# Performance work log

Hardware: AMD Instinct MI355X
Metric: run time of the kernel (lower is better)

Reference implementation:

```python
import jax, jax.numpy as jnp
import numpy as np

D_MODEL = 512
NUM_HEADS = 8
LN_EPS = 1e-5


def _linear(x, W, b):
    # torch nn.Linear: y = x @ W.T + b, W is [out, in]
    return x @ W.T + b


def _layernorm(x, g, b):
    mu = jnp.mean(x, axis=-1, keepdims=True)
    var = jnp.mean((x - mu) ** 2, axis=-1, keepdims=True)
    return (x - mu) * jax.lax.rsqrt(var + LN_EPS) * g + b


def _proj_block(x, W1, b1, ln_g, ln_b, W2, b2):
    # Linear -> LayerNorm -> GELU(exact) -> Linear
    h = _linear(x, W1, b1)
    h = _layernorm(h, ln_g, ln_b)
    h = jax.nn.gelu(h, approximate=False)
    return _linear(h, W2, b2)


def setup_inputs() -> dict:
    key = jax.random.key(0)
    ks = jax.random.split(key, 16)
    d = D_MODEL
    B, N = 32, 50000
    s = 0.02
    inp = {
        "query_features": jax.random.normal(ks[0], (B, d), jnp.float32),
        "candidate_features": jax.random.normal(ks[1], (N, d), jnp.float32),
        # temperature param init: log(1/0.07)
        "temperature": jnp.asarray(np.log(1.0 / 0.07), jnp.float32),
        # query projection
        "qW1": jax.random.normal(ks[2], (d, d), jnp.float32) * s,
        "qb1": jnp.zeros((d,), jnp.float32),
        "q_ln_g": jnp.ones((d,), jnp.float32),
        "q_ln_b": jnp.zeros((d,), jnp.float32),
        "qW2": jax.random.normal(ks[3], (d, d), jnp.float32) * s,
        "qb2": jnp.zeros((d,), jnp.float32),
        # key projection
        "kW1": jax.random.normal(ks[4], (d, d), jnp.float32) * s,
        "kb1": jnp.zeros((d,), jnp.float32),
        "k_ln_g": jnp.ones((d,), jnp.float32),
        "k_ln_b": jnp.zeros((d,), jnp.float32),
        "kW2": jax.random.normal(ks[5], (d, d), jnp.float32) * s,
        "kb2": jnp.zeros((d,), jnp.float32),
        # MultiheadAttention in-proj (only q/k needed for attn weights)
        "in_proj_w": jax.random.normal(ks[6], (3 * d, d), jnp.float32) * s,
        "in_proj_b": jnp.zeros((3 * d,), jnp.float32),
        # similarity fusion MLP: 3 -> 64 -> 1
        "fW1": jax.random.normal(ks[7], (64, 3), jnp.float32) * 0.5,
        "fb1": jnp.zeros((64,), jnp.float32),
        "fW2": jax.random.normal(ks[8], (1, 64), jnp.float32) * 0.5,
        "fb2": jnp.zeros((1,), jnp.float32),
    }
    return inp


def reference(query_features, candidate_features, temperature,
              qW1, qb1, q_ln_g, q_ln_b, qW2, qb2,
              kW1, kb1, k_ln_g, k_ln_b, kW2, kb2,
              in_proj_w, in_proj_b, fW1, fb1, fW2, fb2):
    d = D_MODEL
    H = NUM_HEADS
    dh = d // H

    qp = _proj_block(query_features, qW1, qb1, q_ln_g, q_ln_b, qW2, qb2)      # [B, d]
    kp = _proj_block(candidate_features, kW1, kb1, k_ln_g, k_ln_b, kW2, kb2)  # [N, d]

    # 1) cosine similarity with learnable temperature
    qn = qp / jnp.linalg.norm(qp, axis=-1, keepdims=True)
    kn = kp / jnp.linalg.norm(kp, axis=-1, keepdims=True)
    cosine_sim = (qn @ kn.T) * jnp.exp(temperature)                            # [B, N]

    # 2) euclidean similarity (||q-k|| via quadratic expansion, no [B,N,D] temp)
    q2 = jnp.sum(qp * qp, axis=-1)[:, None]
    k2 = jnp.sum(kp * kp, axis=-1)[None, :]
    d2 = jnp.maximum(q2 + k2 - 2.0 * (qp @ kp.T), 0.0)
    euclidean_sim = 1.0 / (1.0 + jnp.sqrt(d2))                                 # [B, N]

    # 3) attention-weight similarity (torch MHA weights, averaged over heads)
    Wq, Wk = in_proj_w[:d], in_proj_w[d:2 * d]
    bq, bk = in_proj_b[:d], in_proj_b[d:2 * d]
    q = (_linear(qp, Wq, bq)).reshape(-1, H, dh)                               # [B, H, dh]
    k = (_linear(kp, Wk, bk)).reshape(-1, H, dh)                               # [N, H, dh]
    scores = jnp.einsum('bhd,nhd->bhn', q, k) / jnp.sqrt(jnp.float32(dh))      # [B, H, N]
    attn_w = jax.nn.softmax(scores, axis=-1)
    learned_sim = jnp.mean(attn_w, axis=1)                                     # [B, N]

    # fusion MLP over stacked [B, N, 3]
    sims = jnp.stack([cosine_sim, euclidean_sim, learned_sim], axis=-1)
    h = jax.nn.relu(_linear(sims, fW1, fb1))                                   # [B, N, 64]
    out = jax.nn.sigmoid(_linear(h, fW2, fb2))[..., 0]                         # [B, N]
    return out
```

## Files before the change

### kernel.cpp

```cpp
#include <hip/hip_runtime.h>
#include <math.h>

#define D    512
#define BQ   32
#define NH   8
#define MT   64
#define NT   512

typedef _Float16 h2  __attribute__((ext_vector_type(2)));
typedef _Float16 h4v __attribute__((ext_vector_type(4)));
typedef _Float16 h8  __attribute__((ext_vector_type(8)));
typedef float    f4  __attribute__((ext_vector_type(4)));

typedef const __attribute__((address_space(1))) void gas_void;
typedef __attribute__((address_space(3))) void las_void;

__device__ __forceinline__ f4 MF(h8 a, h8 b, f4 c) {
  return __builtin_amdgcn_mfma_f32_16x16x32_f16(a, b, c, 0, 0, 0);
}

__device__ __forceinline__ float erf_fast(float x) {
    float ax = fabsf(x);
    float tt = 1.0f / fmaf(0.3275911f, ax, 1.0f);
    float poly = tt * fmaf(tt, fmaf(tt, fmaf(tt, fmaf(tt, 1.061405429f, -1.453152027f),
                          1.421413741f), -0.284496736f), 0.254829592f);
    float r = 1.0f - poly * __expf(-ax * ax);
    return copysignf(r, x);
}
__device__ __forceinline__ float gelu_fast(float x) {
    return 0.5f * x * (1.0f + erf_fast(x * 0.7071067811865475f));
}
__device__ __forceinline__ float gelu_exact(float x) {
    return 0.5f * x * (1.0f + erff(x * 0.7071067811865475f));
}

__global__ __launch_bounds__(512) void qproj_kernel(
    const float* __restrict__ xq,
    const float* __restrict__ W1, const float* __restrict__ b1,
    const float* __restrict__ lng, const float* __restrict__ lnb,
    const float* __restrict__ W2, const float* __restrict__ b2,
    float* __restrict__ qp,
    float* __restrict__ q2o, float* __restrict__ qinvo,
    _Float16* __restrict__ qph)
{
    __shared__ float xs[D];
    __shared__ float hs[D];
    __shared__ float red[20];
    const int t = threadIdx.x;
    const int row = blockIdx.x;
    const int wave = t >> 6, lane = t & 63;

    xs[t] = xq[row * D + t];
    __syncthreads();

    float a0 = 0.f;
    for (int i = 0; i < D; i += 4) {
        float4 xv = *(const float4*)&xs[i];
        float4 w0 = *(const float4*)&W1[(size_t)t * D + i];
        a0 += xv.x*w0.x + xv.y*w0.y + xv.z*w0.z + xv.w*w0.w;
    }
    float h0 = a0 + b1[t];

    float s1 = h0, s2 = h0 * h0;
    for (int off = 32; off > 0; off >>= 1) { s1 += __shfl_down(s1, off); s2 += __shfl_down(s2, off); }
    if (lane == 0) { red[wave] = s1; red[8 + wave] = s2; }
    __syncthreads();
    if (t == 0) {
        float sa = 0.f, sb = 0.f;
        #pragma unroll
        for (int w = 0; w < 8; ++w) { sa += red[w]; sb += red[8 + w]; }
        float mu = sa / (float)D;
        red[16] = mu;
        red[17] = rsqrtf(sb / (float)D - mu * mu + 1e-5f);
    }
    __syncthreads();
    float mu = red[16], isd = red[17];
    hs[t] = gelu_exact((h0 - mu) * isd * lng[t] + lnb[t]);
    __syncthreads();

    a0 = 0.f;
    for (int i = 0; i < D; i += 4) {
        float4 gv = *(const float4*)&hs[i];
        float4 w0 = *(const float4*)&W2[(size_t)t * D + i];
        a0 += gv.x*w0.x + gv.y*w0.y + gv.z*w0.z + gv.w*w0.w;
    }
    float p0 = a0 + b2[t];
    qp[row * D + t]  = p0;
    qph[row * D + t] = (_Float16)p0;

    s1 = p0 * p0;
    for (int off = 32; off > 0; off >>= 1) s1 += __shfl_down(s1, off);
    if (lane == 0) red[wave] = s1;
    __syncthreads();
    if (t == 0) {
        float sa = 0.f;
        #pragma unroll
        for (int w = 0; w < 8; ++w) sa += red[w];
        q2o[row] = sa;
        qinvo[row] = 1.0f / sqrtf(sa);
    }
}

__global__ __launch_bounds__(256) void wprep_kernel(
    const float* __restrict__ W1, const float* __restrict__ W2,
    _Float16* __restrict__ W1m, _Float16* __restrict__ W2m,
    float* __restrict__ sums)
{
    int idx = blockIdx.x * 256 + threadIdx.x;
    if (blockIdx.x == 0) sums[threadIdx.x] = 0.0f;
    if (idx >= D * D) return;
    W1m[idx] = (_Float16)W1[idx];
    W2m[idx] = (_Float16)W2[idx];
}

__global__ __launch_bounds__(256) void wtld_kernel(
    const float* __restrict__ qp, const float* __restrict__ Wio,
    const float* __restrict__ bio,
    _Float16* __restrict__ Wt)
{
    __shared__ float qpb[D];
    __shared__ float qs[64];
    const int bh = blockIdx.x, b = bh >> 3, h = bh & 7;
    const int t = threadIdx.x;

    qpb[t]       = qp[b * D + t];
    qpb[t + 256] = qp[b * D + t + 256];
    __syncthreads();

    {
        const int d = t >> 2, part = t & 3;
        const float* Wq = Wio + (size_t)(h * 64 + d) * D + part * 128;
        const float* xp = qpb + part * 128;
        float a = 0.f;
        #pragma unroll 8
        for (int i = 0; i < 128; i += 4) {
            float4 xv = *(const float4*)&xp[i];
            float4 wv = *(const float4*)&Wq[i];
            a += xv.x*wv.x + xv.y*wv.y + xv.z*wv.z + xv.w*wv.w;
        }
        a += __shfl_xor(a, 1);
        a += __shfl_xor(a, 2);
        if (part == 0) qs[d] = (a + bio[h * 64 + d]) * 0.125f;
    }
    __syncthreads();

    const float* Wk = Wio + (size_t)D * D + (size_t)(h * 64) * D;
    float a0 = 0.f, a1 = 0.f;
    #pragma unroll 4
    for (int d = 0; d < 64; ++d) {
        float q = qs[d];
        a0 += q * Wk[(size_t)d * D + t];
        a1 += q * Wk[(size_t)d * D + t + 256];
    }
    Wt[(size_t)bh * D + t]       = (_Float16)a0;
    Wt[(size_t)bh * D + t + 256] = (_Float16)a1;
}

__global__ __launch_bounds__(NT) void cand_kernel(
    const float* __restrict__ xc, int N,
    const _Float16* __restrict__ W1m, const _Float16* __restrict__ W2m,
    const float* __restrict__ b1, const float* __restrict__ lng,
    const float* __restrict__ lnb, const float* __restrict__ b2,
    const _Float16* __restrict__ qph,
    const _Float16* __restrict__ Wt,
    const float* __restrict__ q2, const float* __restrict__ qinv,
    const float* __restrict__ tempp,
    float* __restrict__ cosw, float* __restrict__ eucw,
    _Float16* __restrict__ scw, float* __restrict__ sums)
{
    __shared__ _Float16 AH[MT * D];
    __shared__ __align__(16) unsigned char WBUF[65536];
    __shared__ __align__(16) float scr[MT * 33];
    __shared__ float k2p_[8 * MT];
    __shared__ float k2s_[MT], kins_[MT];
    __shared__ float lnmu_[MT], lnisd_[MT];

    float*  dotp_  = scr;
    float2* lnred_ = (float2*)scr;

    const int t    = threadIdx.x;
    const int wave = t >> 6;
    const int lane = t & 63;
    const int l16  = lane & 15;
    const int lK   = lane >> 4;
    const int wcol = wave * 64;
    const int n0   = blockIdx.x * MT;
    const int nvalid = min(MT, N - n0);
    const float expT = expf(tempp[0]);
    const f4 fz = {0.f, 0.f, 0.f, 0.f};

    #pragma unroll
    for (int i = 0; i < 16; ++i) {
        int g = t + NT * i;
        int row = g >> 7;
        int c4 = (g & 127) * 4;
        f4 v = fz;
        if (n0 + row < N)
            v = __builtin_nontemporal_load((const f4*)(xc + (size_t)(n0 + row) * D + c4));
        h4v hi;
        #pragma unroll
        for (int e = 0; e < 4; ++e) hi[e] = (_Float16)v[e];
        *(h4v*)&AH[row * D + (c4 ^ ((row & 7) << 3))] = hi;
    }
    __syncthreads();

    const int sw = (l16 & 7) << 3;

    unsigned rdO[4];
    #pragma unroll
    for (int cb = 0; cb < 4; ++cb) {
        const int col = wcol + cb * 16 + l16;
        rdO[cb] = (unsigned)(col * 64 + ((lK ^ ((col >> 1) & 3)) << 4));
    }
    unsigned dstO[4];
    #pragma unroll
    for (int j = 0; j < 4; ++j) dstO[j] = (unsigned)(wave * 4096 + j * 1024);

    auto gemm = [&](const _Float16* __restrict__ Wm, f4 (&acc)[4][4]) {
        const _Float16* srcB[4];
        #pragma unroll
        for (int j = 0; j < 4; ++j) {
            const int col  = (wave * 4 + j) * 16 + (lane >> 2);
            const int slot = (lane & 3) ^ ((col >> 1) & 3);
            srcB[j] = Wm + (size_t)col * D + slot * 8;
        }
        auto stage = [&](int c, int buf) {
            #pragma unroll
            for (int j = 0; j < 4; ++j)
                __builtin_amdgcn_global_load_lds((gas_void*)(srcB[j] + c * 32),
                    (las_void*)(WBUF + buf * 32768 + dstO[j]), 16, 0, 0);
        };
        auto compute = [&](int c, int buf) {
            const unsigned char* wb = WBUF + buf * 32768;
            h8 bh[4];
            #pragma unroll
            for (int cb = 0; cb < 4; ++cb) bh[cb] = *(const h8*)(wb + rdO[cb]);
            const int ksw = (c * 32 + lK * 8) ^ sw;
            h8 ah[4];
            #pragma unroll
            for (int rb = 0; rb < 4; ++rb)
                ah[rb] = *(const h8*)&AH[(rb * 16 + l16) * D + ksw];
            #pragma unroll
            for (int rb = 0; rb < 4; ++rb)
                #pragma unroll
                for (int cb = 0; cb < 4; ++cb)
                    acc[rb][cb] = MF(ah[rb], bh[cb], acc[rb][cb]);
        };
        stage(0, 0); stage(1, 1);
        #pragma unroll 1
        for (int c = 0; c < 14; ++c) {
            const int buf = c & 1;
            asm volatile("s_waitcnt vmcnt(4)" ::: "memory");
            __builtin_amdgcn_sched_barrier(0);
            compute(c, buf);
            asm volatile("s_waitcnt lgkmcnt(0)" ::: "memory");
            __builtin_amdgcn_sched_barrier(0);
            stage(c + 2, buf);
            __builtin_amdgcn_sched_barrier(0);
        }
        asm volatile("s_waitcnt vmcnt(4)" ::: "memory");
        __builtin_amdgcn_sched_barrier(0);
        compute(14, 0);
        asm volatile("s_waitcnt vmcnt(0)" ::: "memory");
        __builtin_amdgcn_sched_barrier(0);
        compute(15, 1);
    };

    f4 acc[4][4];
    #pragma unroll
    for (int rb = 0; rb < 4; ++rb)
        #pragma unroll
        for (int cb = 0; cb < 4; ++cb) acc[rb][cb] = fz;

    gemm(W1m, acc);

    float s1a[4][4], s2a[4][4];
    #pragma unroll
    for (int rb = 0; rb < 4; ++rb)
        #pragma unroll
        for (int r = 0; r < 4; ++r) { s1a[rb][r] = 0.f; s2a[rb][r] = 0.f; }
    #pragma unroll
    for (int rb = 0; rb < 4; ++rb)
        #pragma unroll
        for (int cb = 0; cb < 4; ++cb) {
            const int j = wcol + cb * 16 + l16;
            const float bb = b1[j];
            #pragma unroll
            for (int r = 0; r < 4; ++r) {
                float v = acc[rb][cb][r] + bb;
                acc[rb][cb][r] = v;
                s1a[rb][r] += v;
                s2a[rb][r] += v * v;
            }
        }
    #pragma unroll
    for (int mm = 1; mm < 16; mm <<= 1)
        #pragma unroll
        for (int rb = 0; rb < 4; ++rb)
            #pragma unroll
            for (int r = 0; r < 4; ++r) {
                s1a[rb][r] += __shfl_xor(s1a[rb][r], mm);
                s2a[rb][r] += __shfl_xor(s2a[rb][r], mm);
            }
    if (l16 == 0) {
        #pragma unroll
        for (int rb = 0; rb < 4; ++rb)
            #pragma unroll
            for (int r = 0; r < 4; ++r)
                lnred_[wave * MT + rb * 16 + lK * 4 + r] = make_float2(s1a[rb][r], s2a[rb][r]);
    }
    __syncthreads();
    if (t < MT) {
        float sa = 0.f, sb = 0.f;
        #pragma unroll
        for (int w = 0; w < 8; ++w) { sa += lnred_[w * MT + t].x; sb += lnred_[w * MT + t].y; }
        float mu = sa * (1.0f / 512.0f);
        float var = sb * (1.0f / 512.0f) - mu * mu;
        lnmu_[t] = mu;
        lnisd_[t] = rsqrtf(var + 1e-5f);
    }
    __syncthreads();

    #pragma unroll
    for (int rb = 0; rb < 4; ++rb)
        #pragma unroll
        for (int cb = 0; cb < 4; ++cb) {
            const int j = wcol + cb * 16 + l16;
            const float gg = lng[j], bb = lnb[j];
            #pragma unroll
            for (int r = 0; r < 4; ++r) {
                const int m = rb * 16 + lK * 4 + r;
                float v = (acc[rb][cb][r] - lnmu_[m]) * lnisd_[m] * gg + bb;
                AH[m * D + (j ^ ((m & 7) << 3))] = (_Float16)gelu_fast(v);
            }
        }
    __syncthreads();

    #pragma unroll
    for (int rb = 0; rb < 4; ++rb)
        #pragma unroll
        for (int cb = 0; cb < 4; ++cb) acc[rb][cb] = fz;
    gemm(W2m, acc);

    float ss[4][4];
    #pragma unroll
    for (int rb = 0; rb < 4; ++rb)
        #pragma unroll
        for (int r = 0; r < 4; ++r) ss[rb][r] = 0.f;
    #pragma unroll
    for (int rb = 0; rb < 4; ++rb)
        #pragma unroll
        for (int cb = 0; cb < 4; ++cb) {
            const int j = wcol + cb * 16 + l16;
            const float bb = b2[j];
            #pragma unroll
            for (int r = 0; r < 4; ++r) {
                float v = acc[rb][cb][r] + bb;
                acc[rb][cb][r] = v;
                ss[rb][r] += v * v;
            }
        }
    #pragma unroll
    for (int mm = 1; mm < 16; mm <<= 1)
        #pragma unroll
        for (int rb = 0; rb < 4; ++rb)
            #pragma unroll
            for (int r = 0; r < 4; ++r)
                ss[rb][r] += __shfl_xor(ss[rb][r], mm);
    __syncthreads();
    if (l16 == 0) {
        #pragma unroll
        for (int rb = 0; rb < 4; ++rb)
            #pragma unroll
            for (int r = 0; r < 4; ++r)
                k2p_[wave * MT + rb * 16 + lK * 4 + r] = ss[rb][r];
    }
    #pragma unroll
    for (int rb = 0; rb < 4; ++rb)
        #pragma unroll
        for (int cb = 0; cb < 4; ++cb) {
            const int j = wcol + cb * 16 + l16;
            #pragma unroll
            for (int r = 0; r < 4; ++r) {
                const int m = rb * 16 + lK * 4 + r;
                AH[m * D + (j ^ ((m & 7) << 3))] = (_Float16)acc[rb][cb][r];
            }
        }
    __syncthreads();

    if (t < MT) {
        float sa = 0.f;
        #pragma unroll
        for (int w = 0; w < 8; ++w) sa += k2p_[w * MT + t];
        k2s_[t] = sa;
        kins_[t] = rsqrtf(fmaxf(sa, 1e-30f));
    }

    f4 as[4][2];
    #pragma unroll
    for (int rb = 0; rb < 4; ++rb) { as[rb][0] = fz; as[rb][1] = fz; }
    {
        const _Float16* wsrcB[2];
        #pragma unroll
        for (int j = 0; j < 2; ++j) {
            const int rr   = j * 16 + (lane >> 2);
            const int slot = (lane & 3) ^ ((rr >> 1) & 3);
            wsrcB[j] = Wt + (size_t)(wave * 32 + rr) * D + slot * 8;
        }
        auto stageWT = [&](int c, int buf) {
            #pragma unroll
            for (int j = 0; j < 2; ++j)
                __builtin_amdgcn_global_load_lds((gas_void*)(wsrcB[j] + c * 32),
                    (las_void*)(WBUF + buf * 16384 + wave * 2048 + j * 1024), 16, 0, 0);
        };
        const unsigned wrd0 = (unsigned)(l16 * 64 + ((lK ^ ((l16 >> 1) & 3)) << 4));
        auto scoreChunk = [&](int c, int buf) {
            const unsigned char* wb = WBUF + buf * 16384 + wave * 2048;
            h8 w0 = *(const h8*)(wb + wrd0);
            h8 w1 = *(const h8*)(wb + 1024 + wrd0);
            const int ksw = (c * 32 + lK * 8) ^ sw;
            #pragma unroll
            for (int rb = 0; rb < 4; ++rb) {
                h8 a = *(const h8*)&AH[(rb * 16 + l16) * D + ksw];
                as[rb][0] = MF(a, w0, as[rb][0]);
                as[rb][1] = MF(a, w1, as[rb][1]);
            }
        };
        stageWT(0, 0); stageWT(1, 1); stageWT(2, 2);
        #pragma unroll 4
        for (int c = 0; c < 12; ++c) {
            asm volatile("s_waitcnt vmcnt(4)" ::: "memory");
            __builtin_amdgcn_sched_barrier(0);
            scoreChunk(c, c & 3);
            asm volatile("s_waitcnt lgkmcnt(0)" ::: "memory");
            __builtin_amdgcn_sched_barrier(0);
            stageWT(c + 3, (c + 3) & 3);
            __builtin_amdgcn_sched_barrier(0);
        }
        asm volatile("s_waitcnt vmcnt(4)" ::: "memory");
        __builtin_amdgcn_sched_barrier(0);
        scoreChunk(12, 0);
        asm volatile("s_waitcnt lgkmcnt(0)" ::: "memory");
        __builtin_amdgcn_sched_barrier(0);
        stageWT(15, 3);
        __builtin_amdgcn_sched_barrier(0);
        asm volatile("s_waitcnt vmcnt(4)" ::: "memory");
        __builtin_amdgcn_sched_barrier(0);
        scoreChunk(13, 1);
        asm volatile("s_waitcnt vmcnt(2)" ::: "memory");
        __builtin_amdgcn_sched_barrier(0);
        scoreChunk(14, 2);
        asm volatile("s_waitcnt vmcnt(0)" ::: "memory");
        __builtin_amdgcn_sched_barrier(0);
        scoreChunk(15, 3);
    }

    {
        #pragma unroll
        for (int cb = 0; cb < 2; ++cb)
            #pragma unroll
            for (int rb = 0; rb < 4; ++rb)
                #pragma unroll
                for (int r = 0; r < 4; ++r)
                    as[rb][cb][r] = __expf(as[rb][cb][r]);
        float part[2] = {0.f, 0.f};
        #pragma unroll
        for (int cb = 0; cb < 2; ++cb)
            #pragma unroll
            for (int rb = 0; rb < 4; ++rb)
                #pragma unroll
                for (int r = 0; r < 4; ++r) {
                    const int n = rb * 16 + lK * 4 + r;
                    if (n < nvalid) part[cb] += as[rb][cb][r];
                }
        #pragma unroll
        for (int cb = 0; cb < 2; ++cb) {
            part[cb] += __shfl_xor(part[cb], 16);
            part[cb] += __shfl_xor(part[cb], 32);
        }
        if (lK == 0) {
            atomicAdd(&sums[wave * 32 + l16], part[0]);
            atomicAdd(&sums[wave * 32 + 16 + l16], part[1]);
        }
    }

    {
        const int rq = wave >> 1, cbq = wave & 1;
        f4 ad = fz;
        const int ra = (rq * 16 + l16) * D;
        const int j = cbq * 16 + l16;
        #pragma unroll 2
        for (int ks = 0; ks < 16; ++ks) {
            const int k0 = ks * 32 + lK * 8;
            const int ksw = k0 ^ sw;
            h8 ah0 = *(const h8*)&AH[ra + ksw];
            h8 bh = *(const h8*)&qph[j * D + k0];
            ad = MF(ah0, bh, ad);
        }
        #pragma unroll
        for (int r = 0; r < 4; ++r)
            dotp_[(rq * 16 + lK * 4 + r) * 33 + cbq * 16 + l16] = ad[r];
    }
    __syncthreads();

    for (int p = t; p < BQ * MT; p += NT) {
        const int m = p & (MT - 1), b = p >> 6;
        if (m < nvalid) {
            float dt = dotp_[m * 33 + b];
            __builtin_nontemporal_store(dt * qinv[b] * kins_[m] * expT,
                                        &cosw[(size_t)b * N + n0 + m]);
            float dd = q2[b] + k2s_[m] - 2.0f * dt;
            __builtin_nontemporal_store(1.0f / (1.0f + sqrtf(fmaxf(dd, 0.f))),
                                        &eucw[(size_t)b * N + n0 + m]);
        }
    }

    _Float16* SC = AH;
    {
        const int bh0 = wave * 32 + l16;
        #pragma unroll
        for (int cb = 0; cb < 2; ++cb) {
            const int bhc = bh0 + cb * 16;
            const int b = bhc >> 3, h = bhc & 7;
            #pragma unroll
            for (int rb = 0; rb < 4; ++rb) {
                #pragma unroll
                for (int r = 0; r < 4; ++r) {
                    const int n = rb * 16 + lK * 4 + r;
                    SC[n * 256 + ((b ^ (n & 31)) * 8) + h] = (_Float16)as[rb][cb][r];
                }
            }
        }
    }
    __syncthreads();

    #pragma unroll
    for (int p = t; p < BQ * MT; p += NT) {
        const int b = p >> 6, n = p & (MT - 1);
        if (n < nvalid) {
            h8 v = *(const h8*)&SC[n * 256 + ((b ^ (n & 31)) * 8)];
            __builtin_nontemporal_store(v, (h8*)&scw[((size_t)b * N + n0 + n) * NH]);
        }
    }
}

__global__ __launch_bounds__(256) void final_kernel(
    const float* __restrict__ cosw, const float* __restrict__ eucw,
    const _Float16* __restrict__ scw, int N,
    const float* __restrict__ sums,
    const float* __restrict__ fW1, const float* __restrict__ fb1,
    const float* __restrict__ fW2, const float* __restrict__ fb2,
    float* __restrict__ out, int total)
{
    __shared__ float w1s[192], b1s[64], w2s[64];
    __shared__ float sis[BQ * NH];
    __shared__ float b2s;
    const int t = threadIdx.x;
    if (t < 192) w1s[t] = fW1[t];
    else { b1s[t - 192] = fb1[t - 192]; w2s[t - 192] = fW2[t - 192]; }
    sis[t] = 0.125f / sums[t];
    if (t == 0) b2s = fb2[0];
    __syncthreads();

    const int idx = blockIdx.x * 256 + t;
    if (idx >= total) return;
    const int b = idx / N;

    float c = cosw[idx], e = eucw[idx];
    h8 v = *(const h8*)&scw[(size_t)idx * NH];
    float ls = 0.f;
    #pragma unroll
    for (int h = 0; h < NH; ++h)
        ls += (float)v[h] * sis[b * NH + h];

    float logit = b2s;
    #pragma unroll
    for (int j = 0; j < 64; ++j) {
        float hj = fmaf(w1s[j*3], c, fmaf(w1s[j*3+1], e, fmaf(w1s[j*3+2], ls, b1s[j])));
        logit = fmaf(w2s[j], fmaxf(hj, 0.f), logit);
    }
    out[idx] = 1.0f / (1.0f + expf(-logit));
}

extern "C" void kernel_launch(void* const* d_in, const int* in_sizes, int n_in,
                              void* d_out, int out_size, void* d_ws, size_t ws_size,
                              hipStream_t stream)
{
    const float* xq   = (const float*)d_in[0];
    const float* xc   = (const float*)d_in[1];
    const float* temp = (const float*)d_in[2];
    const float* qW1  = (const float*)d_in[3];
    const float* qb1  = (const float*)d_in[4];
    const float* qlg  = (const float*)d_in[5];
    const float* qlb  = (const float*)d_in[6];
    const float* qW2  = (const float*)d_in[7];
    const float* qb2  = (const float*)d_in[8];
    const float* kW1  = (const float*)d_in[9];
    const float* kb1  = (const float*)d_in[10];
    const float* klg  = (const float*)d_in[11];
    const float* klb  = (const float*)d_in[12];
    const float* kW2  = (const float*)d_in[13];
    const float* kb2  = (const float*)d_in[14];
    const float* Wio  = (const float*)d_in[15];
    const float* bio  = (const float*)d_in[16];
    const float* fW1  = (const float*)d_in[17];
    const float* fb1  = (const float*)d_in[18];
    const float* fW2  = (const float*)d_in[19];
    const float* fb2  = (const float*)d_in[20];

    const int N = in_sizes[1] / D;

    float* ws   = (float*)d_ws;
    float* qp   = ws;
    float* qv   = qp + BQ * D;
    float* q2   = qv + BQ * D;
    float* qinv = q2 + BQ;
    float* sinv = qinv + BQ;
    float* sums = sinv + BQ * NH;
    float* cosw = sums + BQ * NH;
    float* eucw = cosw + (size_t)BQ * N;
    float* fend = eucw + (size_t)BQ * N;

    _Float16* hb  = (_Float16*)fend;
    _Float16* W1m = hb;
    _Float16* W2m = W1m + D * D;
    _Float16* qph = W2m + D * D;
    _Float16* Wt  = qph + BQ * D;
    _Float16* scw = Wt + BQ * NH * D;

    wprep_kernel<<<(D * D + 255) / 256, 256, 0, stream>>>(kW1, kW2, W1m, W2m, sums);

    qproj_kernel<<<BQ, 512, 0, stream>>>(xq, qW1, qb1, qlg, qlb, qW2, qb2,
                                         qp, q2, qinv, qph);

    wtld_kernel<<<BQ * NH, 256, 0, stream>>>(qp, Wio, bio, Wt);

    const int nblk = (N + MT - 1) / MT;
    cand_kernel<<<nblk, NT, 0, stream>>>(xc, N, W1m, W2m,
                                         kb1, klg, klb, kb2,
                                         qph, Wt, q2, qinv, temp,
                                         cosw, eucw, scw, sums);

    const int total = BQ * N;
    final_kernel<<<(total + 255) / 256, 256, 0, stream>>>(cosw, eucw, scw, N, sums,
                                                          fW1, fb1, fW2, fb2,
                                                          (float*)d_out, total);
}
```

Measured before the change: 311.5 us.

## Enlarge candidate tile from 64 to 80 rows per block

Raises the candidate rows per block from 64 to 80 (five 16-row MFMA blocks), so each block reuses the streamed weight tiles across more rows and the grid has fewer blocks. The LayerNorm and norm reductions are restructured per row-block to keep register pressure in check, and the cosine dot-product work is split into 10 units spread over 8 waves. The cost is more accumulator registers and LDS per block, which may lower occupancy, and the index math now uses a non-power-of-two tile, so it needs divides.

```diff
diff --git a/kernel.cpp b/kernel.cpp
--- a/kernel.cpp
+++ b/kernel.cpp
@@ -4,7 +4,8 @@
 #define D    512
 #define BQ   32
 #define NH   8
-#define MT   64
+#define MT   80
+#define RB   5
 #define NT   512
 
 typedef _Float16 h2  __attribute__((ext_vector_type(2)));
@@ -190,7 +191,7 @@
     const f4 fz = {0.f, 0.f, 0.f, 0.f};
 
     #pragma unroll
-    for (int i = 0; i < 16; ++i) {
+    for (int i = 0; i < 20; ++i) {
         int g = t + NT * i;
         int row = g >> 7;
         int c4 = (g & 127) * 4;
@@ -216,7 +217,7 @@
     #pragma unroll
     for (int j = 0; j < 4; ++j) dstO[j] = (unsigned)(wave * 4096 + j * 1024);
 
-    auto gemm = [&](const _Float16* __restrict__ Wm, f4 (&acc)[4][4]) {
+    auto gemm = [&](const _Float16* __restrict__ Wm, f4 (&acc)[RB][4]) {
         const _Float16* srcB[4];
         #pragma unroll
         for (int j = 0; j < 4; ++j) {
@@ -236,12 +237,12 @@
             #pragma unroll
             for (int cb = 0; cb < 4; ++cb) bh[cb] = *(const h8*)(wb + rdO[cb]);
             const int ksw = (c * 32 + lK * 8) ^ sw;
-            h8 ah[4];
-            #pragma unroll
-            for (int rb = 0; rb < 4; ++rb)
+            h8 ah[RB];
+            #pragma unroll
+            for (int rb = 0; rb < RB; ++rb)
                 ah[rb] = *(const h8*)&AH[(rb * 16 + l16) * D + ksw];
             #pragma unroll
-            for (int rb = 0; rb < 4; ++rb)
+            for (int rb = 0; rb < RB; ++rb)
                 #pragma unroll
                 for (int cb = 0; cb < 4; ++cb)
                     acc[rb][cb] = MF(ah[rb], bh[cb], acc[rb][cb]);
@@ -266,48 +267,41 @@
         compute(15, 1);
     };
 
-    f4 acc[4][4];
-    #pragma unroll
-    for (int rb = 0; rb < 4; ++rb)
+    f4 acc[RB][4];
+    #pragma unroll
+    for (int rb = 0; rb < RB; ++rb)
         #pragma unroll
         for (int cb = 0; cb < 4; ++cb) acc[rb][cb] = fz;
 
     gemm(W1m, acc);
 
-    float s1a[4][4], s2a[4][4];
-    #pragma unroll
-    for (int rb = 0; rb < 4; ++rb)
-        #pragma unroll
-        for (int r = 0; r < 4; ++r) { s1a[rb][r] = 0.f; s2a[rb][r] = 0.f; }
-    #pragma unroll
-    for (int rb = 0; rb < 4; ++rb)
+    #pragma unroll
+    for (int rb = 0; rb < RB; ++rb) {
+        float s1a[4] = {0.f, 0.f, 0.f, 0.f};
+        float s2a[4] = {0.f, 0.f, 0.f, 0.f};
         #pragma unroll
         for (int cb = 0; cb < 4; ++cb) {
-            const int j = wcol + cb * 16 + l16;
-            const float bb = b1[j];
+            const float bb = b1[wcol + cb * 16 + l16];
             #pragma unroll
             for (int r = 0; r < 4; ++r) {
                 float v = acc[rb][cb][r] + bb;
                 acc[rb][cb][r] = v;
-                s1a[rb][r] += v;
-                s2a[rb][r] += v * v;
-            }
-        }
-    #pragma unroll
-    for (int mm = 1; mm < 16; mm <<= 1)
-        #pragma unroll
-        for (int rb = 0; rb < 4; ++rb)
+                s1a[r] += v;
+                s2a[r] += v * v;
+            }
+        }
+        #pragma unroll
+        for (int mm = 1; mm < 16; mm <<= 1)
             #pragma unroll
             for (int r = 0; r < 4; ++r) {
-                s1a[rb][r] += __shfl_xor(s1a[rb][r], mm);
-                s2a[rb][r] += __shfl_xor(s2a[rb][r], mm);
-            }
-    if (l16 == 0) {
-        #pragma unroll
-        for (int rb = 0; rb < 4; ++rb)
+                s1a[r] += __shfl_xor(s1a[r], mm);
+                s2a[r] += __shfl_xor(s2a[r], mm);
+            }
+        if (l16 == 0) {
             #pragma unroll
             for (int r = 0; r < 4; ++r)
-                lnred_[wave * MT + rb * 16 + lK * 4 + r] = make_float2(s1a[rb][r], s2a[rb][r]);
+                lnred_[wave * MT + rb * 16 + lK * 4 + r] = make_float2(s1a[r], s2a[r]);
+        }
     }
     __syncthreads();
     if (t < MT) {
@@ -322,7 +316,7 @@
     __syncthreads();
 
     #pragma unroll
-    for (int rb = 0; rb < 4; ++rb)
+    for (int rb = 0; rb < RB; ++rb)
         #pragma unroll
         for (int cb = 0; cb < 4; ++cb) {
             const int j = wcol + cb * 16 + l16;
@@ -337,46 +331,38 @@
     __syncthreads();
 
     #pragma unroll
-    for (int rb = 0; rb < 4; ++rb)
+    for (int rb = 0; rb < RB; ++rb)
         #pragma unroll
         for (int cb = 0; cb < 4; ++cb) acc[rb][cb] = fz;
     gemm(W2m, acc);
 
-    float ss[4][4];
-    #pragma unroll
-    for (int rb = 0; rb < 4; ++rb)
-        #pragma unroll
-        for (int r = 0; r < 4; ++r) ss[rb][r] = 0.f;
-    #pragma unroll
-    for (int rb = 0; rb < 4; ++rb)
+    #pragma unroll
+    for (int rb = 0; rb < RB; ++rb) {
+        float ss[4] = {0.f, 0.f, 0.f, 0.f};
         #pragma unroll
         for (int cb = 0; cb < 4; ++cb) {
-            const int j = wcol + cb * 16 + l16;
-            const float bb = b2[j];
+            const float bb = b2[wcol + cb * 16 + l16];
             #pragma unroll
             for (int r = 0; r < 4; ++r) {
                 float v = acc[rb][cb][r] + bb;
                 acc[rb][cb][r] = v;
-                ss[rb][r] += v * v;
-            }
-        }
-    #pragma unroll
-    for (int mm = 1; mm < 16; mm <<= 1)
-        #pragma unroll
-        for (int rb = 0; rb < 4; ++rb)
+                ss[r] += v * v;
+            }
+        }
+        #pragma unroll
+        for (int mm = 1; mm < 16; mm <<= 1)
             #pragma unroll
             for (int r = 0; r < 4; ++r)
-                ss[rb][r] += __shfl_xor(ss[rb][r], mm);
-    __syncthreads();
-    if (l16 == 0) {
-        #pragma unroll
-        for (int rb = 0; rb < 4; ++rb)
+                ss[r] += __shfl_xor(ss[r], mm);
+        if (l16 == 0) {
             #pragma unroll
             for (int r = 0; r < 4; ++r)
-                k2p_[wave * MT + rb * 16 + lK * 4 + r] = ss[rb][r];
-    }
-    #pragma unroll
-    for (int rb = 0; rb < 4; ++rb)
+                k2p_[wave * MT + rb * 16 + lK * 4 + r] = ss[r];
+        }
+    }
+    __syncthreads();
+    #pragma unroll
+    for (int rb = 0; rb < RB; ++rb)
         #pragma unroll
         for (int cb = 0; cb < 4; ++cb) {
             const int j = wcol + cb * 16 + l16;
@@ -396,9 +382,9 @@
         kins_[t] = rsqrtf(fmaxf(sa, 1e-30f));
     }
 
-    f4 as[4][2];
-    #pragma unroll
-    for (int rb = 0; rb < 4; ++rb) { as[rb][0] = fz; as[rb][1] = fz; }
+    f4 as[RB][2];
+    #pragma unroll
+    for (int rb = 0; rb < RB; ++rb) { as[rb][0] = fz; as[rb][1] = fz; }
     {
         const _Float16* wsrcB[2];
         #pragma unroll
@@ -420,7 +406,7 @@
             h8 w1 = *(const h8*)(wb + 1024 + wrd0);
             const int ksw = (c * 32 + lK * 8) ^ sw;
             #pragma unroll
-            for (int rb = 0; rb < 4; ++rb) {
+            for (int rb = 0; rb < RB; ++rb) {
                 h8 a = *(const h8*)&AH[(rb * 16 + l16) * D + ksw];
                 as[rb][0] = MF(a, w0, as[rb][0]);
                 as[rb][1] = MF(a, w1, as[rb][1]);
@@ -459,7 +445,7 @@
         #pragma unroll
         for (int cb = 0; cb < 2; ++cb)
             #pragma unroll
-            for (int rb = 0; rb < 4; ++rb)
+            for (int rb = 0; rb < RB; ++rb)
                 #pragma unroll
                 for (int r = 0; r < 4; ++r)
                     as[rb][cb][r] = __expf(as[rb][cb][r]);
@@ -467,7 +453,7 @@
         #pragma unroll
         for (int cb = 0; cb < 2; ++cb)
             #pragma unroll
-            for (int rb = 0; rb < 4; ++rb)
+            for (int rb = 0; rb < RB; ++rb)
                 #pragma unroll
                 for (int r = 0; r < 4; ++r) {
                     const int n = rb * 16 + lK * 4 + r;
@@ -485,26 +471,30 @@
     }
 
     {
-        const int rq = wave >> 1, cbq = wave & 1;
-        f4 ad = fz;
-        const int ra = (rq * 16 + l16) * D;
-        const int j = cbq * 16 + l16;
-        #pragma unroll 2
-        for (int ks = 0; ks < 16; ++ks) {
-            const int k0 = ks * 32 + lK * 8;
-            const int ksw = k0 ^ sw;
-            h8 ah0 = *(const h8*)&AH[ra + ksw];
-            h8 bh = *(const h8*)&qph[j * D + k0];
-            ad = MF(ah0, bh, ad);
-        }
-        #pragma unroll
-        for (int r = 0; r < 4; ++r)
-            dotp_[(rq * 16 + lK * 4 + r) * 33 + cbq * 16 + l16] = ad[r];
+        auto dot_unit = [&](int u) {
+            const int rb = u % RB, cbq = u / RB;
+            f4 ad = fz;
+            const int ra = (rb * 16 + l16) * D;
+            const int j = cbq * 16 + l16;
+            #pragma unroll 2
+            for (int ks = 0; ks < 16; ++ks) {
+                const int k0 = ks * 32 + lK * 8;
+                const int ksw = k0 ^ sw;
+                h8 ah0 = *(const h8*)&AH[ra + ksw];
+                h8 bh = *(const h8*)&qph[j * D + k0];
+                ad = MF(ah0, bh, ad);
+            }
+            #pragma unroll
+            for (int r = 0; r < 4; ++r)
+                dotp_[(rb * 16 + lK * 4 + r) * 33 + cbq * 16 + l16] = ad[r];
+        };
+        dot_unit(wave);
+        if (wave < 2) dot_unit(wave + 8);
     }
     __syncthreads();
 
     for (int p = t; p < BQ * MT; p += NT) {
-        const int m = p & (MT - 1), b = p >> 6;
+        const int b = p / MT, m = p - b * MT;
         if (m < nvalid) {
             float dt = dotp_[m * 33 + b];
             __builtin_nontemporal_store(dt * qinv[b] * kins_[m] * expT,
@@ -523,7 +513,7 @@
             const int bhc = bh0 + cb * 16;
             const int b = bhc >> 3, h = bhc & 7;
             #pragma unroll
-            for (int rb = 0; rb < 4; ++rb) {
+            for (int rb = 0; rb < RB; ++rb) {
                 #pragma unroll
                 for (int r = 0; r < 4; ++r) {
                     const int n = rb * 16 + lK * 4 + r;
@@ -534,9 +524,8 @@
     }
     __syncthreads();
 
-    #pragma unroll
     for (int p = t; p < BQ * MT; p += NT) {
-        const int b = p >> 6, n = p & (MT - 1);
+        const int b = p / MT, n = p - b * MT;
         if (n < nvalid) {
             h8 v = *(const h8*)&SC[n * 256 + ((b ^ (n & 31)) * 8)];
             __builtin_nontemporal_store(v, (h8*)&scw[((size_t)b * N + n0 + n) * NH]);
```

New measurement: 296.1 us. 5.0% less time.
